# Performance work log

Hardware: AMD Instinct MI355X
Metric: run time of the kernel (lower is better)

## Reference

```python
import math
import jax, jax.numpy as jnp
import numpy as np

NH = 2            # n_hashes
BSZ = 128         # bucket size (q_cluster_size == k_cluster_size)
H, E, M = 8, 64, 128   # num_heads, dim_per_head, nb_features
SOFTMAX_TEMP = 1.0 / math.sqrt(E)


def setup_inputs() -> dict:
    rng = jax.random.key(0)
    ks = jax.random.split(rng, 8)
    B, N = 4, 4096
    D = H * E
    return {
        "query": jax.random.normal(ks[0], (B, N, D), jnp.float32),
        "key": jax.random.normal(ks[1], (B, N, D), jnp.float32),
        "value": jax.random.normal(ks[2], (B, N, D), jnp.float32),
        "proj_W": jax.random.normal(ks[3], (M, E), jnp.float32),          # performer random features
        "lsh_alpha": jax.random.normal(ks[4], (E + 2, NH), jnp.float32),  # E2LSH projections (xbox+ adds 2 dims)
        "lsh_beta": jax.random.uniform(ks[5], (1, NH), jnp.float32),      # uniform(0, r=1)
        "out_W": jax.random.normal(ks[6], (E, D), jnp.float32) / math.sqrt(D),
        "out_b": jnp.zeros((E,), jnp.float32),
    }


def _split_heads(x, B, N):
    # b n (h e) -> (b h) n e
    return x.reshape(B, N, H, E).transpose(0, 2, 1, 3).reshape(B * H, N, E)


def _xboxplus(q, k):
    # asymmetric MIPS->L2 transform (XBOXPLUS)
    qn = jnp.linalg.norm(q, axis=-1, keepdims=True)
    kn = jnp.linalg.norm(k, axis=-1, keepdims=True)
    MQ = jnp.max(qn, axis=-2, keepdims=True)
    MK = jnp.max(kn, axis=-2, keepdims=True)
    ext_q = jnp.sqrt(jnp.maximum(MQ ** 2 + MK ** 2 - qn ** 2, 0.0))
    ext_k = jnp.sqrt(jnp.maximum(MQ ** 2 + MK ** 2 - kn ** 2, 0.0))
    q_t = jnp.concatenate([q, ext_q, jnp.zeros_like(qn)], axis=-1)
    k_t = jnp.concatenate([k, jnp.zeros_like(kn), ext_k], axis=-1)
    return q_t, k_t


def _feature_map(x, W, is_query):
    # performer softmax kernel features with separated log-scale
    xt = x * math.sqrt(SOFTMAX_TEMP)
    proj = jnp.einsum('bte,me->btm', xt, W)
    log_phi = proj - 0.5 * jnp.sum(xt * xt, axis=-1, keepdims=True) - 0.5 * math.log(M)
    if is_query:
        stab = jnp.max(log_phi, axis=-1, keepdims=True)           # per-position
    else:
        stab = jnp.max(log_phi, axis=(-1, -2), keepdims=True)     # per-batch
    stab = jax.lax.stop_gradient(stab)
    return jnp.exp(log_phi - stab), stab


def _sort_to_buckets(x, perm):
    # x: (bh, T, d), perm: (NH, bh, T) -> (NH, bh, nbuckets, BSZ, d)
    g = jnp.take_along_axis(x[None], perm[..., None], axis=2)
    nh, bh, T, d = g.shape
    return g.reshape(nh, bh, T // BSZ, BSZ, d)


def reference(query, key, value, proj_W, lsh_alpha, lsh_beta, out_W, out_b):
    B, N, D = query.shape
    q = _split_heads(query, B, N)
    k = _split_heads(key, B, N)
    v = _split_heads(value, B, N)

    # ---- LSH clustering (torch.no_grad in original) ----
    q_t, k_t = _xboxplus(jax.lax.stop_gradient(q), jax.lax.stop_gradient(k))
    q_hash = (q_t @ lsh_alpha + lsh_beta).transpose(2, 0, 1)   # (NH, bh, N)
    k_hash = (k_t @ lsh_alpha + lsh_beta).transpose(2, 0, 1)
    q_pos = jnp.argsort(q_hash, axis=-1)
    k_pos = jnp.argsort(k_hash, axis=-1)

    # ---- Performer linear-attention branch ----
    q_prime, q_ls = _feature_map(q, proj_W, True)
    k_prime, k_ls = _feature_map(k, proj_W, False)
    prime_log_scale = q_ls + k_ls                               # (bh, N, 1)

    qk1 = jnp.einsum('btm,bm->bt', q_prime, k_prime.sum(axis=1))        # normalization
    kv = jnp.einsum('bsm,bsd->bmd', k_prime, v)
    qkv = jnp.einsum('btm,bmd->btd', q_prime, kv)

    # ---- bucketed exact attention correction ----
    s_q = _sort_to_buckets(q, q_pos)
    s_k = _sort_to_buckets(k, k_pos)
    s_v = _sort_to_buckets(v, k_pos)
    s_qp = _sort_to_buckets(q_prime, q_pos)
    s_kp = _sort_to_buckets(k_prime, k_pos)
    s_pls = _sort_to_buckets(prime_log_scale, q_pos)            # (NH, bh, nb, BSZ, 1)

    inner = jnp.einsum('hbnie,hbnje->hbnij', s_q, s_k) * SOFTMAX_TEMP
    dots_prime = jnp.einsum('hbnim,hbnjm->hbnij', s_qp, s_kp)

    q_rev = jnp.argsort(q_pos, axis=-1)
    if NH > 1:
        k_rev = jnp.argsort(k_pos, axis=-1)
        q_bidx = (q_rev // BSZ).transpose(1, 2, 0)  # (bh, N, NH)
        k_bidx = (k_rev // BSZ).transpose(1, 2, 0)
        s_qb = _sort_to_buckets(q_bidx, q_pos)      # (NH, bh, nb, BSZ, NH)
        s_kb = _sort_to_buckets(k_bidx, k_pos)
        dup = jnp.sum(s_qb[..., :, None, :] == s_kb[..., None, :, :], axis=-1).astype(inner.dtype)
        inner = inner - jnp.log(dup)
        dots_prime = dots_prime / dup

    dots_lse = jnp.maximum(jnp.max(inner, axis=-1, keepdims=True), s_pls)
    dots = jnp.exp(inner - dots_lse) - dots_prime * jnp.exp(s_pls - dots_lse)
    dots_sum = dots.sum(axis=-1, keepdims=True)
    so = jnp.einsum('hbnij,hbnjd->hbnid', dots, s_v)

    def unsort(s_x):
        nh, bh, nb, bsz, d = s_x.shape
        return jnp.take_along_axis(s_x.reshape(nh, bh, nb * bsz, d), q_rev[..., None], axis=2)

    o = unsort(so)
    logits = unsort(dots_lse)          # (NH, bh, N, 1)
    dots_sum_u = unsort(dots_sum)

    norm_ls = jax.nn.logsumexp(logits, axis=0)                  # (bh, N, 1)
    probs = jnp.exp(logits - norm_ls[None])
    out_lsh = jnp.sum(o * probs, axis=0)
    prime_scale = jnp.exp(prime_log_scale - norm_ls)
    out = out_lsh + qkv * prime_scale
    normalization = (dots_sum_u * probs).sum(axis=0) + qk1[..., None] * prime_scale
    out_n = out / jnp.maximum(normalization, 1e-6)

    out_n = out_n.reshape(B, H, N, E).transpose(0, 2, 1, 3).reshape(B, N, H * E)
    return out_n @ out_W.T + out_b
```

## Files before the change

### kernel.cpp

```cpp
#include <hip/hip_runtime.h>
#include <math.h>

#define BH 32
#define NSEQ 4096
#define EDIM 64
#define MDIM 128
#define NHASH 2
#define NBUCK 32
#define BSZC 128
#define BB 4
#define HH 8
#define DD 512
#define NCHUNK 16

static constexpr size_t OFF_SQQ  = 0;
static constexpr size_t SZ_ROWD  = (size_t)BH*NSEQ*8;
static constexpr size_t OFF_SQK  = OFF_SQQ + SZ_ROWD;
static constexpr size_t OFF_QH   = OFF_SQK + SZ_ROWD;
static constexpr size_t SZ_HASH  = (size_t)NHASH*BH*NSEQ*8;
static constexpr size_t OFF_KH   = OFF_QH + SZ_HASH;
static constexpr size_t OFF_MAXQ = OFF_KH + SZ_HASH;
static constexpr size_t OFF_MAXK = OFF_MAXQ + 256;
static constexpr size_t OFF_KLS  = OFF_MAXK + 256;
static constexpr size_t OFF_QPOS = OFF_KLS + 256;
static constexpr size_t SZ_POS   = (size_t)NHASH*BH*NSEQ*4;
static constexpr size_t OFF_KPOS = OFF_QPOS + SZ_POS;
static constexpr size_t OFF_QREV = OFF_KPOS + SZ_POS;
static constexpr size_t OFF_KREV = OFF_QREV + SZ_POS;
static constexpr size_t OFF_QP   = OFF_KREV + SZ_POS;
static constexpr size_t SZ_PRIME = (size_t)BH*NSEQ*MDIM*4;
static constexpr size_t OFF_KP   = OFF_QP + SZ_PRIME;
static constexpr size_t OFF_QLS  = OFF_KP + SZ_PRIME;
static constexpr size_t OFF_KV   = OFF_QLS + (size_t)BH*NSEQ*4;
static constexpr size_t OFF_KSUM = OFF_KV + (size_t)BH*MDIM*EDIM*4;
static constexpr size_t OFF_O    = OFF_KSUM + (size_t)BH*MDIM*4;
static constexpr size_t OFF_LSE  = OFF_O + (size_t)NHASH*BH*NSEQ*EDIM*4;
static constexpr size_t OFF_DSUM = OFF_LSE + (size_t)NHASH*BH*NSEQ*4;
static constexpr size_t OFF_OUTN = OFF_DSUM + (size_t)NHASH*BH*NSEQ*4;
static constexpr size_t OFF_PKV  = OFF_OUTN + (size_t)BB*NSEQ*DD*4;
static constexpr size_t OFF_PKS  = OFF_PKV + (size_t)BH*NCHUNK*MDIM*EDIM*4;
static constexpr size_t OFF_PROJ = OFF_PKV;
static constexpr size_t OFF_KPB  = OFF_OUTN;
static constexpr size_t OFF_VB   = OFF_PKV;

#define SQRT_TEMP 0.3535533905932738f
#define HALF_LOG_M 2.4260151319598085f
#define LN2F 0.6931471805599453f

typedef __bf16 bf16_t;
typedef bf16_t bf16x8 __attribute__((ext_vector_type(8)));
typedef bf16_t bf16x4 __attribute__((ext_vector_type(4)));
typedef float  f32x16_t __attribute__((ext_vector_type(16)));
#define Z16 {0.f,0.f,0.f,0.f,0.f,0.f,0.f,0.f,0.f,0.f,0.f,0.f,0.f,0.f,0.f,0.f}

__device__ __forceinline__ unsigned encF(float f){
  unsigned u = __float_as_uint(f);
  return (u & 0x80000000u) ? ~u : (u | 0x80000000u);
}
__device__ __forceinline__ float decF(unsigned e){
  return __uint_as_float((e & 0x80000000u) ? (e ^ 0x80000000u) : ~e);
}

__global__ void k_init(char* __restrict__ ws){
  int idx = blockIdx.x*256 + threadIdx.x;
  if (idx < BH){
    ((unsigned long long*)(ws+OFF_MAXQ))[idx] = 0ull;
    ((unsigned long long*)(ws+OFF_MAXK))[idx] = 0ull;
    ((unsigned*)(ws+OFF_KLS))[idx] = encF(-INFINITY);
  }
}

__global__ __launch_bounds__(256) void k_sumsq(const float* __restrict__ q, const float* __restrict__ k,
                                               const float* __restrict__ alpha, char* __restrict__ ws){
  int p = blockIdx.x*256 + threadIdx.x;
  int bh = p >> 12, t = p & (NSEQ-1);
  int bo = bh >> 3, hh = bh & 7;
  const float* qr = q + ((size_t)bo*NSEQ + t)*DD + hh*EDIM;
  const float* kr = k + ((size_t)bo*NSEQ + t)*DD + hh*EDIM;
  double sq = 0.0, sk = 0.0, a0 = 0.0, a1 = 0.0, c0 = 0.0, c1 = 0.0;
  for (int e4 = 0; e4 < EDIM; e4 += 4){
    float4 qv4 = *(const float4*)(qr + e4);
    float4 kv4 = *(const float4*)(kr + e4);
    float qs[4] = {qv4.x, qv4.y, qv4.z, qv4.w};
    float ks[4] = {kv4.x, kv4.y, kv4.z, kv4.w};
    #pragma unroll
    for (int j = 0; j < 4; j++){
      double a = qs[j], b = ks[j];
      double al0 = alpha[(e4+j)*2+0], al1 = alpha[(e4+j)*2+1];
      sq = fma(a, a, sq);  sk = fma(b, b, sk);
      a0 = fma(a, al0, a0); a1 = fma(a, al1, a1);
      c0 = fma(b, al0, c0); c1 = fma(b, al1, c1);
    }
  }
  ((double*)(ws+OFF_SQQ))[p] = sq;
  ((double*)(ws+OFF_SQK))[p] = sk;
  double* proj = (double*)(ws+OFF_PROJ);
  proj[p]                       = a0;
  proj[(size_t)BH*NSEQ   + p]   = a1;
  proj[(size_t)BH*NSEQ*2 + p]   = c0;
  proj[(size_t)BH*NSEQ*3 + p]   = c1;
  int lane = threadIdx.x & 63, wid = threadIdx.x >> 6;
  double mq = sq, mk = sk;
  for (int o = 32; o; o >>= 1){ mq = fmax(mq, __shfl_xor(mq, o)); mk = fmax(mk, __shfl_xor(mk, o)); }
  __shared__ double smq[4], smk[4];
  if (!lane){ smq[wid] = mq; smk[wid] = mk; }
  __syncthreads();
  if (!threadIdx.x){
    double a = fmax(fmax(smq[0], smq[1]), fmax(smq[2], smq[3]));
    double b = fmax(fmax(smk[0], smk[1]), fmax(smk[2], smk[3]));
    atomicMax((unsigned long long*)(ws+OFF_MAXQ) + bh, (unsigned long long)__double_as_longlong(a));
    atomicMax((unsigned long long*)(ws+OFF_MAXK) + bh, (unsigned long long)__double_as_longlong(b));
  }
}

__global__ __launch_bounds__(256) void k_hash(const float* __restrict__ alpha, const float* __restrict__ beta,
                                              char* __restrict__ ws){
  int p = blockIdx.x*256 + threadIdx.x;
  int bh = p >> 12;
  double mqk = ((const double*)(ws+OFF_MAXQ))[bh] + ((const double*)(ws+OFF_MAXK))[bh];
  double sq  = ((const double*)(ws+OFF_SQQ))[p];
  double sk  = ((const double*)(ws+OFF_SQK))[p];
  double extq = sqrt(fmax(mqk - sq, 0.0));
  double extk = sqrt(fmax(mqk - sk, 0.0));
  const double* proj = (const double*)(ws+OFF_PROJ);
  double a0 = proj[p];
  double a1 = proj[(size_t)BH*NSEQ   + p];
  double c0 = proj[(size_t)BH*NSEQ*2 + p];
  double c1 = proj[(size_t)BH*NSEQ*3 + p];
  a0 += extq * (double)alpha[64*2+0]; a1 += extq * (double)alpha[64*2+1];
  c0 += extk * (double)alpha[65*2+0]; c1 += extk * (double)alpha[65*2+1];
  double b0 = beta[0], b1 = beta[1];
  double* qh = (double*)(ws+OFF_QH);
  double* kh = (double*)(ws+OFF_KH);
  qh[p] = a0 + b0; qh[(size_t)BH*NSEQ + p] = a1 + b1;
  kh[p] = c0 + b0; kh[(size_t)BH*NSEQ + p] = c1 + b1;
}

__global__ __launch_bounds__(1024) void k_sort(char* __restrict__ ws){
  int row = blockIdx.x;
  bool isK = row >= NHASH*BH;
  int r = isK ? row - NHASH*BH : row;
  const double* hash = (const double*)(ws + (isK ? OFF_KH : OFF_QH)) + (size_t)r*NSEQ;
  int* pos = (int*)(ws + (isK ? OFF_KPOS : OFF_QPOS)) + (size_t)r*NSEQ;
  int* rev = (int*)(ws + (isK ? OFF_KREV : OFF_QREV)) + (size_t)r*NSEQ;
  __shared__ double ks_[NSEQ];
  __shared__ int    is_[NSEQ];
  int tid = threadIdx.x, lane = tid & 63;

  double key[4]; int idx[4];
  #pragma unroll
  for (int m = 0; m < 4; m++){ int i = m*1024 + tid; key[m] = hash[i]; idx[m] = i; }

  #pragma unroll
  for (int k = 2; k <= 64; k <<= 1){
    #pragma unroll
    for (int j = 32; j > 0; j >>= 1){
      if (j > (k >> 1)) continue;
      #pragma unroll
      for (int m = 0; m < 4; m++){
        int i = m*1024 + tid;
        bool up = ((i & k) == 0);
        double pk = __shfl_xor(key[m], j);
        int    pi = __shfl_xor(idx[m], j);
        bool isLower = ((lane & j) == 0);
        double lo = isLower ? key[m] : pk;
        double hi = isLower ? pk : key[m];
        if ((lo > hi) == up){ key[m] = pk; idx[m] = pi; }
      }
    }
  }
  #pragma unroll
  for (int m = 0; m < 4; m++){ int i = m*1024 + tid; ks_[i] = key[m]; is_[i] = idx[m]; }
  __syncthreads();

  for (int k = 128; k <= NSEQ; k <<= 1){
    for (int j = k >> 1; j >= 64; j >>= 1){
      for (int i = tid; i < NSEQ; i += 1024){
        int ixj = i ^ j;
        if (ixj > i){
          double a = ks_[i], b = ks_[ixj];
          bool up = ((i & k) == 0);
          if ((a > b) == up){
            ks_[i] = b; ks_[ixj] = a;
            int tmp = is_[i]; is_[i] = is_[ixj]; is_[ixj] = tmp;
          }
        }
      }
      __syncthreads();
    }
    #pragma unroll
    for (int m = 0; m < 4; m++){ int i = m*1024 + tid; key[m] = ks_[i]; idx[m] = is_[i]; }
    #pragma unroll
    for (int j = 32; j > 0; j >>= 1){
      #pragma unroll
      for (int m = 0; m < 4; m++){
        int i = m*1024 + tid;
        bool up = ((i & k) == 0);
        double pk = __shfl_xor(key[m], j);
        int    pi = __shfl_xor(idx[m], j);
        bool isLower = ((lane & j) == 0);
        double lo = isLower ? key[m] : pk;
        double hi = isLower ? pk : key[m];
        if ((lo > hi) == up){ key[m] = pk; idx[m] = pi; }
      }
    }
    #pragma unroll
    for (int m = 0; m < 4; m++){ int i = m*1024 + tid; ks_[i] = key[m]; is_[i] = idx[m]; }
    __syncthreads();
  }
  for (int i = tid; i < NSEQ; i += 1024){ int t = is_[i]; pos[i] = t; rev[t] = i; }
}

__global__ __launch_bounds__(256) void k_feat(const float* __restrict__ query, const float* __restrict__ key,
                                              const float* __restrict__ projW, char* __restrict__ ws){
  int tid = threadIdx.x, lane = tid & 63, wid = tid >> 6;
  __shared__ __align__(16) float s_x[4][16][EDIM];
  float* qp  = (float*)(ws+OFF_QP);
  float* qls = (float*)(ws+OFF_QLS);
  float* kp  = (float*)(ws+OFF_KP);
  const float* w0p = projW + (size_t)lane*EDIM;
  const float* w1p = projW + (size_t)(64+lane)*EDIM;

  {
    float ss[16];
    #pragma unroll
    for (int it = 0; it < 16; it++){
      int p = blockIdx.x*64 + wid*16 + it;
      int bh = p >> 12, t = p & (NSEQ-1), bo = bh >> 3, hh = bh & 7;
      float xv = query[((size_t)bo*NSEQ + t)*DD + hh*EDIM + lane] * SQRT_TEMP;
      s_x[wid][it][lane] = xv;
      float s = xv*xv;
      for (int o = 32; o; o >>= 1) s += __shfl_xor(s, o);
      ss[it] = s;
    }
    float a0[16], a1[16];
    #pragma unroll
    for (int it = 0; it < 16; it++){ a0[it] = 0.f; a1[it] = 0.f; }
    #pragma unroll 1
    for (int e4 = 0; e4 < 16; e4++){
      float4 w0 = *(const float4*)(w0p + e4*4);
      float4 w1 = *(const float4*)(w1p + e4*4);
      #pragma unroll
      for (int it = 0; it < 16; it++){
        float4 sx = *(const float4*)&s_x[wid][it][e4*4];
        a0[it] = fmaf(sx.x, w0.x, a0[it]);
        a1[it] = fmaf(sx.x, w1.x, a1[it]);
        a0[it] = fmaf(sx.y, w0.y, a0[it]);
        a1[it] = fmaf(sx.y, w1.y, a1[it]);
        a0[it] = fmaf(sx.z, w0.z, a0[it]);
        a1[it] = fmaf(sx.z, w1.z, a1[it]);
        a0[it] = fmaf(sx.w, w0.w, a0[it]);
        a1[it] = fmaf(sx.w, w1.w, a1[it]);
      }
    }
    #pragma unroll
    for (int it = 0; it < 16; it++){
      int p = blockIdx.x*64 + wid*16 + it;
      float c = 0.5f*ss[it] + HALF_LOG_M;
      float lp0 = a0[it] - c, lp1 = a1[it] - c;
      float mx = fmaxf(lp0, lp1);
      for (int o = 32; o; o >>= 1) mx = fmaxf(mx, __shfl_xor(mx, o));
      size_t base = (size_t)p*MDIM;
      qp[base + lane]      = expf(lp0 - mx);
      qp[base + 64 + lane] = expf(lp1 - mx);
      if (!lane) qls[p] = mx;
    }
  }

  int bh0 = (blockIdx.x*64) >> 12;
  float bmax = -INFINITY;
  {
    float ss[16];
    #pragma unroll
    for (int it = 0; it < 16; it++){
      int p = blockIdx.x*64 + wid*16 + it;
      int bh = p >> 12, t = p & (NSEQ-1), bo = bh >> 3, hh = bh & 7;
      float xv = key[((size_t)bo*NSEQ + t)*DD + hh*EDIM + lane] * SQRT_TEMP;
      s_x[wid][it][lane] = xv;
      float s = xv*xv;
      for (int o = 32; o; o >>= 1) s += __shfl_xor(s, o);
      ss[it] = s;
    }
    float a0[16], a1[16];
    #pragma unroll
    for (int it = 0; it < 16; it++){ a0[it] = 0.f; a1[it] = 0.f; }
    #pragma unroll 1
    for (int e4 = 0; e4 < 16; e4++){
      float4 w0 = *(const float4*)(w0p + e4*4);
      float4 w1 = *(const float4*)(w1p + e4*4);
      #pragma unroll
      for (int it = 0; it < 16; it++){
        float4 sx = *(const float4*)&s_x[wid][it][e4*4];
        a0[it] = fmaf(sx.x, w0.x, a0[it]);
        a1[it] = fmaf(sx.x, w1.x, a1[it]);
        a0[it] = fmaf(sx.y, w0.y, a0[it]);
        a1[it] = fmaf(sx.y, w1.y, a1[it]);
        a0[it] = fmaf(sx.z, w0.z, a0[it]);
        a1[it] = fmaf(sx.z, w1.z, a1[it]);
        a0[it] = fmaf(sx.w, w0.w, a0[it]);
        a1[it] = fmaf(sx.w, w1.w, a1[it]);
      }
    }
    #pragma unroll
    for (int it = 0; it < 16; it++){
      int p = blockIdx.x*64 + wid*16 + it;
      float c = 0.5f*ss[it] + HALF_LOG_M;
      float lp0 = a0[it] - c, lp1 = a1[it] - c;
      size_t base = (size_t)p*MDIM;
      kp[base + lane]      = lp0;
      kp[base + 64 + lane] = lp1;
      float mx = fmaxf(lp0, lp1);
      for (int o = 32; o; o >>= 1) mx = fmaxf(mx, __shfl_xor(mx, o));
      bmax = fmaxf(bmax, mx);
    }
  }
  __shared__ float wm[4];
  if (!lane) wm[wid] = bmax;
  __syncthreads();
  if (!tid){
    float m = fmaxf(fmaxf(wm[0], wm[1]), fmaxf(wm[2], wm[3]));
    atomicMax((unsigned*)(ws+OFF_KLS) + bh0, encF(m));
  }
}

__global__ __launch_bounds__(256, 4) void k_kv(const float* __restrict__ value, char* __restrict__ ws){
  int b = blockIdx.x >> 4;
  int chunk = blockIdx.x & 15;
  int bo = b >> 3, hh = b & 7;
  const float* kp = (const float*)(ws+OFF_KP) + (size_t)b*NSEQ*MDIM;
  float stab = decF(((const unsigned*)(ws+OFF_KLS))[b]);
  __shared__ float skp[32][MDIM];
  __shared__ float sv [32][EDIM];
  int tid = threadIdx.x;
  int d = tid & 63, mg = tid >> 6;
  int m0 = mg*32;
  float acc[32];
  #pragma unroll
  for (int i = 0; i < 32; i++) acc[i] = 0.f;
  float ksacc = 0.f;
  #pragma unroll 1
  for (int s0 = chunk*256; s0 < chunk*256 + 256; s0 += 32){
    __syncthreads();
    {
      const float4* src = (const float4*)(kp + (size_t)s0*MDIM);
      #pragma unroll
      for (int l = tid; l < 32*MDIM/4; l += 256){
        float4 x = src[l];
        x.x = expf(x.x - stab); x.y = expf(x.y - stab);
        x.z = expf(x.z - stab); x.w = expf(x.w - stab);
        ((float4*)skp)[l] = x;
      }
    }
    #pragma unroll
    for (int l = tid; l < 32*EDIM/4; l += 256){
      int r = l >> 4, c4 = (l & 15) << 2;
      *(float4*)&sv[r][c4] = *(const float4*)(value + ((size_t)bo*NSEQ + s0 + r)*DD + hh*EDIM + c4);
    }
    __syncthreads();
    #pragma unroll 1
    for (int ss = 0; ss < 32; ss += 2){
      float vv0 = sv[ss+0][d];
      float vv1 = sv[ss+1][d];
      #pragma unroll
      for (int mq = 0; mq < 8; mq++){
        float4 k0 = *(const float4*)&skp[ss+0][m0 + mq*4];
        float4 k1 = *(const float4*)&skp[ss+1][m0 + mq*4];
        acc[mq*4+0] = fmaf(k0.x, vv0, acc[mq*4+0]);
        acc[mq*4+1] = fmaf(k0.y, vv0, acc[mq*4+1]);
        acc[mq*4+2] = fmaf(k0.z, vv0, acc[mq*4+2]);
        acc[mq*4+3] = fmaf(k0.w, vv0, acc[mq*4+3]);
        acc[mq*4+0] = fmaf(k1.x, vv1, acc[mq*4+0]);
        acc[mq*4+1] = fmaf(k1.y, vv1, acc[mq*4+1]);
        acc[mq*4+2] = fmaf(k1.z, vv1, acc[mq*4+2]);
        acc[mq*4+3] = fmaf(k1.w, vv1, acc[mq*4+3]);
      }
    }
    if (tid < 128){
      #pragma unroll
      for (int ss = 0; ss < 32; ss++) ksacc += skp[ss][tid];
    }
  }
  float* pkv = (float*)(ws+OFF_PKV) + ((size_t)(b*NCHUNK + chunk)*MDIM + m0)*EDIM + d;
  #pragma unroll
  for (int mi = 0; mi < 32; mi++) pkv[mi*EDIM] = acc[mi];
  if (tid < 128)
    ((float*)(ws+OFF_PKS))[(b*NCHUNK + chunk)*MDIM + tid] = ksacc;
}

__global__ __launch_bounds__(256) void k_kvred(char* __restrict__ ws){
  int blk = blockIdx.x;
  if (blk < 1024){
    int idx = blk*256 + threadIdx.x;
    int b = idx >> 13, rem = idx & 8191;
    const float* pkv = (const float*)(ws+OFF_PKV);
    float s = 0.f;
    #pragma unroll
    for (int c = 0; c < NCHUNK; c++) s += pkv[(((size_t)b*NCHUNK + c) << 13) + rem];
    ((float*)(ws+OFF_KV))[idx] = s;
  } else {
    int j = (blk - 1024)*256 + threadIdx.x;
    const float* pks = (const float*)(ws+OFF_PKS);
    int b = j >> 7, m = j & 127;
    float s = 0.f;
    #pragma unroll
    for (int c = 0; c < NCHUNK; c++) s += pks[(b*NCHUNK + c)*MDIM + m];
    ((float*)(ws+OFF_KSUM))[j] = s;
  }
}

__global__ __launch_bounds__(256) void k_cvt(const float* __restrict__ value, char* __restrict__ ws){
  int blk = blockIdx.x;
  if (blk < 16384){
    size_t idx = (size_t)blk*256 + threadIdx.x;
    const float4* kp = (const float4*)(ws+OFF_KP);
    bf16_t* kpb = (bf16_t*)(ws+OFF_KPB);
    int b = (int)(idx >> 17);
    float stab = decF(((const unsigned*)(ws+OFF_KLS))[b]);
    float4 v = kp[idx];
    v.x = expf(v.x - stab); v.y = expf(v.y - stab);
    v.z = expf(v.z - stab); v.w = expf(v.w - stab);
    *(bf16x4*)(kpb + idx*4) = (bf16x4){(bf16_t)v.x,(bf16_t)v.y,(bf16_t)v.z,(bf16_t)v.w};
  } else {
    bf16_t* vb = (bf16_t*)(ws+OFF_VB);
    size_t idx = (size_t)(blk - 16384)*256 + threadIdx.x;
    int e4 = (int)(idx & 15) << 2;
    int t  = (int)((idx >> 4) & 4095);
    int b  = (int)(idx >> 16);
    int bo = b >> 3, hh = b & 7;
    float4 x = *(const float4*)(value + ((size_t)bo*NSEQ + t)*DD + hh*EDIM + e4);
    *(bf16x4*)(vb + ((size_t)b*NSEQ + t)*EDIM + e4) =
        (bf16x4){(bf16_t)x.x,(bf16_t)x.y,(bf16_t)x.z,(bf16_t)x.w};
  }
}

__global__ __launch_bounds__(256, 2) void k_bucket(const float* __restrict__ query,
                                                   const float* __restrict__ key,
                                                   char* __restrict__ ws){
  __shared__ __align__(16) bf16_t s_kT[128*72];
  __shared__ __align__(16) bf16_t s_kp[128*136];
  __shared__ __align__(16) bf16_t s_v [64*136];
  __shared__ int   s_tq[128], s_tk[128], s_qb[128], s_kb[128];
  __shared__ float s_pls[128];

  int blk = blockIdx.x;
  int h = blk >> 10;
  int b = (blk >> 5) & 31;
  int n = blk & 31;
  int tid = threadIdx.x, lane = tid & 63, wid = tid >> 6;
  int col = lane & 31, half = lane >> 5;
  int bo = b >> 3, hh = b & 7;

  const int* kpos  = (const int*)(ws+OFF_KPOS) + ((size_t)h*BH + b)*NSEQ + n*BSZC;
  const int* qpos  = (const int*)(ws+OFF_QPOS) + ((size_t)h*BH + b)*NSEQ + n*BSZC;
  const int* qrev0 = (const int*)(ws+OFF_QREV) + (size_t)b*NSEQ;
  const int* qrev1 = (const int*)(ws+OFF_QREV) + ((size_t)BH + b)*NSEQ;
  const int* krev0 = (const int*)(ws+OFF_KREV) + (size_t)b*NSEQ;
  const int* krev1 = (const int*)(ws+OFF_KREV) + ((size_t)BH + b)*NSEQ;
  const float* qp_g = (const float*)(ws+OFF_QP) + (size_t)b*NSEQ*MDIM;
  const bf16_t* kpb_g = (const bf16_t*)(ws+OFF_KPB) + (size_t)b*NSEQ*MDIM;
  const bf16_t* vb_g  = (const bf16_t*)(ws+OFF_VB)  + (size_t)b*NSEQ*EDIM;
  const float* qls  = (const float*)(ws+OFF_QLS) + (size_t)b*NSEQ;
  float klsb = decF(((const unsigned*)(ws+OFF_KLS))[b]);

  if (tid < 128){
    int t = qpos[tid];
    s_tq[tid]  = t;
    s_pls[tid] = qls[t] + klsb;
    s_qb[tid]  = (qrev0[t] >> 7) | ((qrev1[t] >> 7) << 16);
  } else {
    int j = tid - 128;
    int t = kpos[j];
    s_tk[j] = t;
    s_kb[j] = (krev0[t] >> 7) | ((krev1[t] >> 7) << 16);
  }
  __syncthreads();

  int mrow = wid*32 + col;
  int tq_m = s_tq[mrow];
  const float* qr  = query + ((size_t)bo*NSEQ + tq_m)*DD + hh*EDIM + half*8;
  const float* qpr = qp_g + (size_t)tq_m*MDIM + half*8;
  float4 aqf[8];
  #pragma unroll
  for (int kb = 0; kb < 4; kb++){
    aqf[2*kb]   = *(const float4*)(qr + kb*16);
    aqf[2*kb+1] = *(const float4*)(qr + kb*16 + 4);
  }
  float4 aqpf[16];
  #pragma unroll
  for (int kb = 0; kb < 8; kb++){
    aqpf[2*kb]   = *(const float4*)(qpr + kb*16);
    aqpf[2*kb+1] = *(const float4*)(qpr + kb*16 + 4);
  }

  for (int l = tid; l < 128*16; l += 256){
    int j = l >> 4, e4 = (l & 15) << 2;
    int t = s_tk[j];
    float4 x = *(const float4*)(key + ((size_t)bo*NSEQ + t)*DD + hh*EDIM + e4);
    bf16x4 y = {(bf16_t)x.x, (bf16_t)x.y, (bf16_t)x.z, (bf16_t)x.w};
    *(bf16x4*)&s_kT[j*72 + e4] = y;
  }
  for (int l = tid; l < 128*16; l += 256){
    int j = l >> 4, m8 = (l & 15) << 3;
    int t = s_tk[j];
    *(bf16x8*)&s_kp[j*136 + m8] = *(const bf16x8*)(kpb_g + (size_t)t*MDIM + m8);
  }
  for (int l = tid; l < 128*8; l += 256){
    int j = l >> 3, d8 = (l & 7) << 3;
    int t = s_tk[j];
    bf16x8 vv = *(const bf16x8*)(vb_g + (size_t)t*EDIM + d8);
    #pragma unroll
    for (int i = 0; i < 8; i++) s_v[(d8+i)*136 + j] = vv[i];
  }
  __syncthreads();

  float* o_g   = (float*)(ws+OFF_O)    + ((size_t)h*BH + b)*NSEQ*EDIM;
  float* lse_g = (float*)(ws+OFF_LSE)  + ((size_t)h*BH + b)*NSEQ;
  float* dsm_g = (float*)(ws+OFF_DSUM) + ((size_t)h*BH + b)*NSEQ;

  bf16x8 aq[4];
  #pragma unroll
  for (int kb = 0; kb < 4; kb++){
    float4 x0 = aqf[2*kb], x1 = aqf[2*kb+1];
    aq[kb] = (bf16x8){(bf16_t)x0.x,(bf16_t)x0.y,(bf16_t)x0.z,(bf16_t)x0.w,
                      (bf16_t)x1.x,(bf16_t)x1.y,(bf16_t)x1.z,(bf16_t)x1.w};
  }
  f32x16_t ain[4] = {Z16, Z16, Z16, Z16};
  #pragma unroll
  for (int jt = 0; jt < 4; jt++){
    #pragma unroll
    for (int kb = 0; kb < 4; kb++){
      bf16x8 bk = *(const bf16x8*)&s_kT[(jt*32 + col)*72 + kb*16 + half*8];
      ain[jt] = __builtin_amdgcn_mfma_f32_32x32x16_bf16(aq[kb], bk, ain[jt], 0, 0, 0);
    }
  }

  bf16x8 aqp[8];
  #pragma unroll
  for (int kb = 0; kb < 8; kb++){
    float4 x0 = aqpf[2*kb], x1 = aqpf[2*kb+1];
    aqp[kb] = (bf16x8){(bf16_t)x0.x,(bf16_t)x0.y,(bf16_t)x0.z,(bf16_t)x0.w,
                       (bf16_t)x1.x,(bf16_t)x1.y,(bf16_t)x1.z,(bf16_t)x1.w};
  }
  f32x16_t apr[4] = {Z16, Z16, Z16, Z16};
  #pragma unroll
  for (int jt = 0; jt < 4; jt++){
    #pragma unroll
    for (int kb = 0; kb < 8; kb++){
      bf16x8 bk = *(const bf16x8*)&s_kp[(jt*32 + col)*136 + kb*16 + half*8];
      apr[jt] = __builtin_amdgcn_mfma_f32_32x32x16_bf16(aqp[kb], bk, apr[jt], 0, 0, 0);
    }
  }
  __syncthreads();

  float pls_r[16]; int qb_r[16];
  #pragma unroll
  for (int i = 0; i < 16; i++){
    int r = wid*32 + (i & 3) + 8*(i >> 2) + 4*half;
    pls_r[i] = s_pls[r];
    qb_r[i]  = s_qb[r];
  }
  float mx[16];
  #pragma unroll
  for (int i = 0; i < 16; i++) mx[i] = -INFINITY;
  #pragma unroll
  for (int jt = 0; jt < 4; jt++){
    int kbp = s_kb[jt*32 + col];
    int kb0 = kbp & 0xffff, kb1 = kbp >> 16;
    #pragma unroll
    for (int i = 0; i < 16; i++){
      int dup2 = ((qb_r[i] & 0xffff) == kb0) & ((qb_r[i] >> 16) == kb1);
      float in = ain[jt][i]*0.125f - (dup2 ? LN2F : 0.0f);
      float dp = dup2 ? apr[jt][i]*0.5f : apr[jt][i];
      ain[jt][i] = in; apr[jt][i] = dp;
      mx[i] = fmaxf(mx[i], in);
    }
  }
  #pragma unroll
  for (int i = 0; i < 16; i++){
    #pragma unroll
    for (int o = 16; o; o >>= 1) mx[i] = fmaxf(mx[i], __shfl_xor(mx[i], o));
  }
  float L[16], eps[16], dsum[16];
  #pragma unroll
  for (int i = 0; i < 16; i++){
    L[i] = fmaxf(mx[i], pls_r[i]);
    eps[i] = expf(pls_r[i] - L[i]);
    dsum[i] = 0.f;
  }
  #pragma unroll
  for (int jt = 0; jt < 4; jt++){
    #pragma unroll
    for (int i = 0; i < 16; i++){
      float d = expf(ain[jt][i] - L[i]) - apr[jt][i]*eps[i];
      dsum[i] += d;
      int r = wid*32 + (i & 3) + 8*(i >> 2) + 4*half;
      s_kp[r*136 + jt*32 + col] = (bf16_t)d;
    }
  }
  #pragma unroll
  for (int i = 0; i < 16; i++){
    #pragma unroll
    for (int o = 16; o; o >>= 1) dsum[i] += __shfl_xor(dsum[i], o);
  }
  __syncthreads();

  f32x16_t ao[2] = {Z16, Z16};
  #pragma unroll
  for (int kb = 0; kb < 8; kb++){
    bf16x8 ad = *(const bf16x8*)&s_kp[mrow*136 + kb*16 + half*8];
    #pragma unroll
    for (int dt = 0; dt < 2; dt++){
      bf16x8 bv = *(const bf16x8*)&s_v[(dt*32 + col)*136 + kb*16 + half*8];
      ao[dt] = __builtin_amdgcn_mfma_f32_32x32x16_bf16(ad, bv, ao[dt], 0, 0, 0);
    }
  }

  #pragma unroll
  for (int i = 0; i < 16; i++){
    int r = wid*32 + (i & 3) + 8*(i >> 2) + 4*half;
    int t = s_tq[r];
    o_g[(size_t)t*EDIM + col]      = ao[0][i];
    o_g[(size_t)t*EDIM + 32 + col] = ao[1][i];
    if (col == 0){ lse_g[t] = L[i]; dsm_g[t] = dsum[i]; }
  }
}

__global__ __launch_bounds__(256) void k_combine(char* __restrict__ ws){
  int b = blockIdx.x >> 6;
  int chunk = blockIdx.x & 63;
  int tid = threadIdx.x, lane = tid & 63, wid = tid >> 6;
  __shared__ float s_kv[MDIM*EDIM];
  __shared__ float s_ks[MDIM];
  __shared__ float s_qp[4][MDIM];
  const float* kv = (const float*)(ws+OFF_KV) + (size_t)b*MDIM*EDIM;
  for (int l = tid; l < MDIM*EDIM; l += 256) s_kv[l] = kv[l];
  if (tid < MDIM) s_ks[tid] = ((const float*)(ws+OFF_KSUM))[b*MDIM + tid];
  __syncthreads();
  const float* qp_g  = (const float*)(ws+OFF_QP) + (size_t)b*NSEQ*MDIM;
  const float* qls   = (const float*)(ws+OFF_QLS) + (size_t)b*NSEQ;
  const float* lse_g = (const float*)(ws+OFF_LSE);
  const float* dsm_g = (const float*)(ws+OFF_DSUM);
  const float* o_g   = (const float*)(ws+OFF_O);
  float* outn = (float*)(ws+OFF_OUTN);
  float klsb = decF(((const unsigned*)(ws+OFF_KLS))[b]);
  int bo = b >> 3, hh = b & 7;
  for (int it = 0; it < 16; it++){
    int t = chunk*64 + wid*16 + it;
    float qp0 = qp_g[(size_t)t*MDIM + lane];
    float qp1 = qp_g[(size_t)t*MDIM + 64 + lane];
    s_qp[wid][lane] = qp0; s_qp[wid][64 + lane] = qp1;
    float qkv = 0.f;
    for (int m = 0; m < 128; m++) qkv = fmaf(s_qp[wid][m], s_kv[m*64 + lane], qkv);
    float qk1 = qp0*s_ks[lane] + qp1*s_ks[64 + lane];
    for (int o = 32; o; o >>= 1) qk1 += __shfl_xor(qk1, o);
    size_t pidx = (size_t)b*NSEQ + t;
    float l0 = lse_g[pidx], l1 = lse_g[(size_t)BH*NSEQ + pidx];
    float mx = fmaxf(l0, l1);
    float nls = mx + logf(expf(l0 - mx) + expf(l1 - mx));
    float p0 = expf(l0 - nls), p1 = expf(l1 - nls);
    float ps = expf(qls[t] + klsb - nls);
    float o0 = o_g[pidx*EDIM + lane];
    float o1 = o_g[((size_t)BH*NSEQ + pidx)*EDIM + lane];
    float ds0 = dsm_g[pidx], ds1 = dsm_g[(size_t)BH*NSEQ + pidx];
    float outv = o0*p0 + o1*p1 + qkv*ps;
    float nrm  = ds0*p0 + ds1*p1 + qk1*ps;
    outn[((size_t)bo*NSEQ + t)*DD + hh*EDIM + lane] = outv / fmaxf(nrm, 1e-6f);
  }
}

__global__ __launch_bounds__(256) void k_final(const float* __restrict__ outW, const float* __restrict__ outB,
                                               const char* __restrict__ ws, float* __restrict__ out){
  __shared__ float WT[DD*65];
  __shared__ float s_x[4][DD];
  int tid = threadIdx.x, lane = tid & 63, wid = tid >> 6;
  for (int l = tid; l < EDIM*DD; l += 256){
    int e = l >> 9, d = l & 511;
    WT[d*65 + e] = outW[l];
  }
  __syncthreads();
  const float* outn = (const float*)(ws+OFF_OUTN);
  for (int it = 0; it < 16; it++){
    int p = blockIdx.x*64 + wid*16 + it;
    const float* x = outn + (size_t)p*DD;
    #pragma unroll
    for (int c = 0; c < 8; c++) s_x[wid][c*64 + lane] = x[c*64 + lane];
    float acc = 0.f;
    for (int d = 0; d < DD; d++) acc = fmaf(s_x[wid][d], WT[d*65 + lane], acc);
    out[(size_t)p*EDIM + lane] = acc + outB[lane];
  }
}

extern "C" void kernel_launch(void* const* d_in, const int* in_sizes, int n_in,
                              void* d_out, int out_size, void* d_ws, size_t ws_size,
                              hipStream_t stream) {
  const float* query = (const float*)d_in[0];
  const float* key   = (const float*)d_in[1];
  const float* value = (const float*)d_in[2];
  const float* projW = (const float*)d_in[3];
  const float* alpha = (const float*)d_in[4];
  const float* beta  = (const float*)d_in[5];
  const float* outW  = (const float*)d_in[6];
  const float* outB  = (const float*)d_in[7];
  char* ws = (char*)d_ws;
  float* out = (float*)d_out;

  k_init <<<1,    256, 0, stream>>>(ws);
  k_sumsq<<<512,  256, 0, stream>>>(query, key, alpha, ws);
  k_hash <<<512,  256, 0, stream>>>(alpha, beta, ws);
  k_sort <<<128, 1024, 0, stream>>>(ws);
  k_feat <<<2048, 256, 0, stream>>>(query, key, projW, ws);
  k_kv   <<<512,  256, 0, stream>>>(value, ws);
  k_kvred<<<1040, 256, 0, stream>>>(ws);
  k_cvt  <<<24576,256, 0, stream>>>(value, ws);
  k_bucket<<<2048,256, 0, stream>>>(query, key, ws);
  k_combine<<<2048,256,0, stream>>>(ws);
  k_final<<<256,  256, 0, stream>>>(outW, outB, ws, out);
}
```

Before: 684.0 us.

## Fuse key-feature bf16 conversion into k_kv and register-block combine's qkv matvec

The k_kv kernel, which already computes exp(kp - stab) for each tile, now also writes the bf16 copy of the key features. The key part of k_cvt is removed, so that separate pass no longer re-reads the fp32 features and recomputes the exponentials. k_combine now stages a transposed kv matrix and all 16 query feature rows per wave in shared memory, then computes the 16 qkv dot products together with float4 loads. This replaces the previous per-position serialized reload and scalar inner loop, at the cost of more shared memory and registers per block.

```diff
diff --git a/kernel.cpp b/kernel.cpp
--- a/kernel.cpp
+++ b/kernel.cpp
@@ -328,6 +328,7 @@
   int chunk = blockIdx.x & 15;
   int bo = b >> 3, hh = b & 7;
   const float* kp = (const float*)(ws+OFF_KP) + (size_t)b*NSEQ*MDIM;
+  bf16_t* kpb = (bf16_t*)(ws+OFF_KPB) + (size_t)b*NSEQ*MDIM;
   float stab = decF(((const unsigned*)(ws+OFF_KLS))[b]);
   __shared__ float skp[32][MDIM];
   __shared__ float sv [32][EDIM];
@@ -349,6 +350,8 @@
         x.x = expf(x.x - stab); x.y = expf(x.y - stab);
         x.z = expf(x.z - stab); x.w = expf(x.w - stab);
         ((float4*)skp)[l] = x;
+        *(bf16x4*)(kpb + (size_t)(s0 + (l >> 5))*MDIM + ((l & 31) << 2)) =
+            (bf16x4){(bf16_t)x.x,(bf16_t)x.y,(bf16_t)x.z,(bf16_t)x.w};
       }
     }
     #pragma unroll
@@ -409,28 +412,15 @@
 }
 
 __global__ __launch_bounds__(256) void k_cvt(const float* __restrict__ value, char* __restrict__ ws){
-  int blk = blockIdx.x;
-  if (blk < 16384){
-    size_t idx = (size_t)blk*256 + threadIdx.x;
-    const float4* kp = (const float4*)(ws+OFF_KP);
-    bf16_t* kpb = (bf16_t*)(ws+OFF_KPB);
-    int b = (int)(idx >> 17);
-    float stab = decF(((const unsigned*)(ws+OFF_KLS))[b]);
-    float4 v = kp[idx];
-    v.x = expf(v.x - stab); v.y = expf(v.y - stab);
-    v.z = expf(v.z - stab); v.w = expf(v.w - stab);
-    *(bf16x4*)(kpb + idx*4) = (bf16x4){(bf16_t)v.x,(bf16_t)v.y,(bf16_t)v.z,(bf16_t)v.w};
-  } else {
-    bf16_t* vb = (bf16_t*)(ws+OFF_VB);
-    size_t idx = (size_t)(blk - 16384)*256 + threadIdx.x;
-    int e4 = (int)(idx & 15) << 2;
-    int t  = (int)((idx >> 4) & 4095);
-    int b  = (int)(idx >> 16);
-    int bo = b >> 3, hh = b & 7;
-    float4 x = *(const float4*)(value + ((size_t)bo*NSEQ + t)*DD + hh*EDIM + e4);
-    *(bf16x4*)(vb + ((size_t)b*NSEQ + t)*EDIM + e4) =
-        (bf16x4){(bf16_t)x.x,(bf16_t)x.y,(bf16_t)x.z,(bf16_t)x.w};
-  }
+  bf16_t* vb = (bf16_t*)(ws+OFF_VB);
+  size_t idx = (size_t)blockIdx.x*256 + threadIdx.x;
+  int e4 = (int)(idx & 15) << 2;
+  int t  = (int)((idx >> 4) & 4095);
+  int b  = (int)(idx >> 16);
+  int bo = b >> 3, hh = b & 7;
+  float4 x = *(const float4*)(value + ((size_t)bo*NSEQ + t)*DD + hh*EDIM + e4);
+  *(bf16x4*)(vb + ((size_t)b*NSEQ + t)*EDIM + e4) =
+      (bf16x4){(bf16_t)x.x,(bf16_t)x.y,(bf16_t)x.z,(bf16_t)x.w};
 }
 
 __global__ __launch_bounds__(256, 2) void k_bucket(const float* __restrict__ query,
@@ -629,14 +619,22 @@
   int b = blockIdx.x >> 6;
   int chunk = blockIdx.x & 63;
   int tid = threadIdx.x, lane = tid & 63, wid = tid >> 6;
-  __shared__ float s_kv[MDIM*EDIM];
+  __shared__ __align__(16) float s_kvT[EDIM*132];
   __shared__ float s_ks[MDIM];
-  __shared__ float s_qp[4][MDIM];
+  __shared__ __align__(16) float s_qp[4][16][MDIM];
   const float* kv = (const float*)(ws+OFF_KV) + (size_t)b*MDIM*EDIM;
-  for (int l = tid; l < MDIM*EDIM; l += 256) s_kv[l] = kv[l];
+  for (int l = tid; l < MDIM*EDIM; l += 256){
+    int m = l >> 6, e = l & 63;
+    s_kvT[e*132 + m] = kv[l];
+  }
   if (tid < MDIM) s_ks[tid] = ((const float*)(ws+OFF_KSUM))[b*MDIM + tid];
-  __syncthreads();
   const float* qp_g  = (const float*)(ws+OFF_QP) + (size_t)b*NSEQ*MDIM;
+  int t0 = chunk*64 + wid*16;
+  for (int l = lane; l < 16*32; l += 64){
+    int it = l >> 5, m4 = l & 31;
+    *(float4*)&s_qp[wid][it][m4*4] = *(const float4*)(qp_g + (size_t)(t0+it)*MDIM + m4*4);
+  }
+  __syncthreads();
   const float* qls   = (const float*)(ws+OFF_QLS) + (size_t)b*NSEQ;
   const float* lse_g = (const float*)(ws+OFF_LSE);
   const float* dsm_g = (const float*)(ws+OFF_DSUM);
@@ -644,13 +642,28 @@
   float* outn = (float*)(ws+OFF_OUTN);
   float klsb = decF(((const unsigned*)(ws+OFF_KLS))[b]);
   int bo = b >> 3, hh = b & 7;
+
+  float qkv[16];
+  #pragma unroll
+  for (int it = 0; it < 16; it++) qkv[it] = 0.f;
+  #pragma unroll 1
+  for (int m4 = 0; m4 < 32; m4++){
+    float4 kv4 = *(const float4*)&s_kvT[lane*132 + m4*4];
+    #pragma unroll
+    for (int it = 0; it < 16; it++){
+      float4 q4 = *(const float4*)&s_qp[wid][it][m4*4];
+      qkv[it] = fmaf(q4.x, kv4.x, qkv[it]);
+      qkv[it] = fmaf(q4.y, kv4.y, qkv[it]);
+      qkv[it] = fmaf(q4.z, kv4.z, qkv[it]);
+      qkv[it] = fmaf(q4.w, kv4.w, qkv[it]);
+    }
+  }
+
+  #pragma unroll 1
   for (int it = 0; it < 16; it++){
-    int t = chunk*64 + wid*16 + it;
-    float qp0 = qp_g[(size_t)t*MDIM + lane];
-    float qp1 = qp_g[(size_t)t*MDIM + 64 + lane];
-    s_qp[wid][lane] = qp0; s_qp[wid][64 + lane] = qp1;
-    float qkv = 0.f;
-    for (int m = 0; m < 128; m++) qkv = fmaf(s_qp[wid][m], s_kv[m*64 + lane], qkv);
+    int t = t0 + it;
+    float qp0 = s_qp[wid][it][lane];
+    float qp1 = s_qp[wid][it][64 + lane];
     float qk1 = qp0*s_ks[lane] + qp1*s_ks[64 + lane];
     for (int o = 32; o; o >>= 1) qk1 += __shfl_xor(qk1, o);
     size_t pidx = (size_t)b*NSEQ + t;
@@ -662,7 +675,7 @@
     float o0 = o_g[pidx*EDIM + lane];
     float o1 = o_g[((size_t)BH*NSEQ + pidx)*EDIM + lane];
     float ds0 = dsm_g[pidx], ds1 = dsm_g[(size_t)BH*NSEQ + pidx];
-    float outv = o0*p0 + o1*p1 + qkv*ps;
+    float outv = o0*p0 + o1*p1 + qkv[it]*ps;
     float nrm  = ds0*p0 + ds1*p1 + qk1*ps;
     outn[((size_t)bo*NSEQ + t)*DD + hh*EDIM + lane] = outv / fmaxf(nrm, 1e-6f);
   }
@@ -711,7 +724,7 @@
   k_feat <<<2048, 256, 0, stream>>>(query, key, projW, ws);
   k_kv   <<<512,  256, 0, stream>>>(value, ws);
   k_kvred<<<1040, 256, 0, stream>>>(ws);
-  k_cvt  <<<24576,256, 0, stream>>>(value, ws);
+  k_cvt  <<<8192, 256, 0, stream>>>(value, ws);
   k_bucket<<<2048,256, 0, stream>>>(query, key, ws);
   k_combine<<<2048,256,0, stream>>>(ws);
   k_final<<<256,  256, 0, stream>>>(outW, outB, ws, out);
```

After: 665.2 us. 2.8% less time.
